# Performance work log

Hardware: AMD Instinct MI355X
Metric: run time of the kernel (lower is better)

Reference implementation:

```python
import jax, jax.numpy as jnp
import numpy as np


def setup_inputs() -> dict:
    key = jax.random.key(0)
    k1, k2, k3, k4 = jax.random.split(key, 4)
    N = 100000          # n_users + n_items nodes
    E = 1600000         # nonzeros in normalized adjacency (avg degree 16)
    D = 64              # embedding dim
    edge_row = jnp.sort(jax.random.randint(k1, (E,), 0, N, dtype=jnp.int32))
    edge_col = jax.random.randint(k2, (E,), 0, N, dtype=jnp.int32)
    edge_val = jax.random.uniform(k3, (E,), dtype=jnp.float32)
    embeds = jax.random.normal(k4, (N, D), dtype=jnp.float32)
    return {
        "edge_row": edge_row,
        "edge_col": edge_col,
        "edge_val": edge_val,
        "embeds": embeds,
        "num_nodes": N,
    }


def reference(edge_row, edge_col, edge_val, embeds, num_nodes):
    # out = A @ embeds, A given in COO: A[row[e], col[e]] = val[e]
    gathered = edge_val[:, None] * embeds[edge_col]        # [E, D]
    out = jax.ops.segment_sum(gathered, edge_row, num_segments=num_nodes)  # [N, D]
    return out
```

## Files before the change

kernel.cpp:

```cpp
#include <hip/hip_runtime.h>


#define GCN_D 64

typedef float f4 __attribute__((ext_vector_type(4)));

__global__ __launch_bounds__(256) void quant_kernel(
    const float* __restrict__ embeds,
    unsigned char* __restrict__ ebq,
    float* __restrict__ scale,
    int N)
{
    const int t   = blockIdx.x * blockDim.x + threadIdx.x;
    const int row = t >> 3;
    if (row >= N) return;
    const int l8 = (threadIdx.x & 7) * 8;

    const f4 a = __builtin_nontemporal_load(
        (const f4*)(embeds + (size_t)row * GCN_D + l8));
    const f4 b = __builtin_nontemporal_load(
        (const f4*)(embeds + (size_t)row * GCN_D + l8 + 4));

    float m = fmaxf(fmaxf(fmaxf(fabsf(a.x), fabsf(a.y)),
                          fmaxf(fabsf(a.z), fabsf(a.w))),
                    fmaxf(fmaxf(fabsf(b.x), fabsf(b.y)),
                          fmaxf(fabsf(b.z), fabsf(b.w))));
    m = fmaxf(m, __shfl_xor(m, 1));
    m = fmaxf(m, __shfl_xor(m, 2));
    m = fmaxf(m, __shfl_xor(m, 4));

    const float inv = (m > 0.f) ? 127.f / m : 0.f;
    const int q0 = (int)rintf(fminf(fmaxf(a.x * inv, -127.f), 127.f)) + 128;
    const int q1 = (int)rintf(fminf(fmaxf(a.y * inv, -127.f), 127.f)) + 128;
    const int q2 = (int)rintf(fminf(fmaxf(a.z * inv, -127.f), 127.f)) + 128;
    const int q3 = (int)rintf(fminf(fmaxf(a.w * inv, -127.f), 127.f)) + 128;
    const int q4 = (int)rintf(fminf(fmaxf(b.x * inv, -127.f), 127.f)) + 128;
    const int q5 = (int)rintf(fminf(fmaxf(b.y * inv, -127.f), 127.f)) + 128;
    const int q6 = (int)rintf(fminf(fmaxf(b.z * inv, -127.f), 127.f)) + 128;
    const int q7 = (int)rintf(fminf(fmaxf(b.w * inv, -127.f), 127.f)) + 128;

    unsigned int p0 =
        (unsigned)q0 | ((unsigned)q1 << 8) | ((unsigned)q2 << 16) | ((unsigned)q3 << 24);
    unsigned int p1 =
        (unsigned)q4 | ((unsigned)q5 << 8) | ((unsigned)q6 << 16) | ((unsigned)q7 << 24);

    unsigned int* dst = (unsigned int*)(ebq + (size_t)row * GCN_D + l8);
    dst[0] = p0;
    dst[1] = p1;
    if ((threadIdx.x & 7) == 0) scale[row] = m * (1.f / 127.f);
}

__global__ __launch_bounds__(256) void edge_kernel(
    const int* __restrict__ edge_row,
    const int* __restrict__ edge_col,
    const float* __restrict__ edge_val,
    const float* __restrict__ scale,
    int* __restrict__ row_ptr,
    int2* __restrict__ pw,
    int E, int N)
{
    const int e = blockIdx.x * blockDim.x + threadIdx.x;
    if (e >= E) return;
    const int r    = edge_row[e];
    const int prev = (e == 0) ? -1 : edge_row[e - 1];
    for (int k = prev + 1; k <= r; ++k) row_ptr[k] = e;
    if (e == E - 1)
        for (int k = r + 1; k <= N; ++k) row_ptr[k] = E;

    const int   c = edge_col[e];
    const float w = edge_val[e] * scale[c];
    pw[e] = make_int2(c, __float_as_int(w));
}

__device__ __forceinline__ void q8_fma4(unsigned int g, float w, f4& acc) {
    acc.x += w * (float)( g        & 0xffu);
    acc.y += w * (float)((g >> 8)  & 0xffu);
    acc.z += w * (float)((g >> 16) & 0xffu);
    acc.w += w * (float)( g >> 24);
}

__global__ __launch_bounds__(256) void gcn_row_q8_kernel(
    const int* __restrict__ row_ptr,
    const int2* __restrict__ pw,
    const unsigned char* __restrict__ ebq,
    float* __restrict__ out,
    int N)
{
    const int tid = blockIdx.x * blockDim.x + threadIdx.x;
    const int row = tid >> 4;
    if (row >= N) return;
    const int db = (threadIdx.x & 15) * 4;

    const int p0 = row_ptr[row];
    const int p1 = row_ptr[row + 1];

    f4    acc = (f4)0.0f;
    float ws  = 0.0f;

    if (p1 > p0) {
        const int nb = (p1 - p0 + 7) >> 3;
        int k = p0;

        int      cA[8], cB[8];
        float    wA[8], wB[8];
        unsigned gA[8], gB[8];

        auto LOAD = [&](int kk, int* c, float* w, unsigned* g) {
            #pragma unroll
            for (int j = 0; j < 8; ++j) {
                const int idx = (kk + j < p1) ? (kk + j) : (p1 - 1);
                const int2 t  = pw[idx];
                c[j] = t.x;
                w[j] = (kk + j < p1) ? __int_as_float(t.y) : 0.0f;
            }
            #pragma unroll
            for (int j = 0; j < 8; ++j)
                g[j] = *(const unsigned*)(ebq + (size_t)c[j] * GCN_D + db);
        };
        auto COMP = [&](const float* w, const unsigned* g) {
            #pragma unroll
            for (int j = 0; j < 8; ++j) {
                q8_fma4(g[j], w[j], acc);
                ws += w[j];
            }
        };

        LOAD(k, cA, wA, gA); k += 8;
        int b = 1;
        for (; b + 1 < nb; b += 2) {
            LOAD(k, cB, wB, gB); k += 8;
            COMP(wA, gA);
            LOAD(k, cA, wA, gA); k += 8;
            COMP(wB, gB);
        }
        if (b < nb) {
            LOAD(k, cB, wB, gB);
            COMP(wA, gA);
            COMP(wB, gB);
        } else {
            COMP(wA, gA);
        }
    }

    acc = acc - 128.0f * ws;
    __builtin_nontemporal_store(acc, (f4*)(out + (size_t)row * GCN_D + db));
}

extern "C" void kernel_launch(void* const* d_in, const int* in_sizes, int n_in,
                              void* d_out, int out_size, void* d_ws, size_t ws_size,
                              hipStream_t stream) {
    const int*   edge_row = (const int*)d_in[0];
    const int*   edge_col = (const int*)d_in[1];
    const float* edge_val = (const float*)d_in[2];
    const float* embeds   = (const float*)d_in[3];
    float*       out      = (float*)d_out;

    const int E = in_sizes[0];
    const int N = out_size / GCN_D;

    int* row_ptr = (int*)d_ws;
    const size_t sc_off = (((size_t)(N + 1) * 4) + 255) & ~(size_t)255;
    float* scale = (float*)((char*)d_ws + sc_off);
    const size_t pw_off = ((sc_off + (size_t)N * 4) + 255) & ~(size_t)255;
    int2* pw = (int2*)((char*)d_ws + pw_off);
    const size_t q_off = ((pw_off + (size_t)E * 8) + 255) & ~(size_t)255;
    unsigned char* ebq = (unsigned char*)d_ws + q_off;

    const int quant_blocks = (N * 8 + 255) / 256;
    quant_kernel<<<quant_blocks, 256, 0, stream>>>(embeds, ebq, scale, N);

    const int edge_blocks = (E + 255) / 256;
    edge_kernel<<<edge_blocks, 256, 0, stream>>>(
        edge_row, edge_col, edge_val, scale, row_ptr, pw, E, N);

    const int row_blocks = (N * 16 + 255) / 256;
    gcn_row_q8_kernel<<<row_blocks, 256, 0, stream>>>(
        row_ptr, pw, ebq, out, N);
}
```

Before: 139.6 us.

## Switch gather table from int8 to bf16 and fuse prep kernels

```diff
diff --git a/kernel.cpp b/kernel.cpp
--- a/kernel.cpp
+++ b/kernel.cpp
@@ -4,137 +4,114 @@
 #define GCN_D 64
 
 typedef float f4 __attribute__((ext_vector_type(4)));
+typedef unsigned int u2 __attribute__((ext_vector_type(2)));
+typedef unsigned int uv4 __attribute__((ext_vector_type(4)));
 
-__global__ __launch_bounds__(256) void quant_kernel(
-    const float* __restrict__ embeds,
-    unsigned char* __restrict__ ebq,
-    float* __restrict__ scale,
-    int N)
-{
-    const int t   = blockIdx.x * blockDim.x + threadIdx.x;
-    const int row = t >> 3;
-    if (row >= N) return;
-    const int l8 = (threadIdx.x & 7) * 8;
-
-    const f4 a = __builtin_nontemporal_load(
-        (const f4*)(embeds + (size_t)row * GCN_D + l8));
-    const f4 b = __builtin_nontemporal_load(
-        (const f4*)(embeds + (size_t)row * GCN_D + l8 + 4));
-
-    float m = fmaxf(fmaxf(fmaxf(fabsf(a.x), fabsf(a.y)),
-                          fmaxf(fabsf(a.z), fabsf(a.w))),
-                    fmaxf(fmaxf(fabsf(b.x), fabsf(b.y)),
-                          fmaxf(fabsf(b.z), fabsf(b.w))));
-    m = fmaxf(m, __shfl_xor(m, 1));
-    m = fmaxf(m, __shfl_xor(m, 2));
-    m = fmaxf(m, __shfl_xor(m, 4));
-
-    const float inv = (m > 0.f) ? 127.f / m : 0.f;
-    const int q0 = (int)rintf(fminf(fmaxf(a.x * inv, -127.f), 127.f)) + 128;
-    const int q1 = (int)rintf(fminf(fmaxf(a.y * inv, -127.f), 127.f)) + 128;
-    const int q2 = (int)rintf(fminf(fmaxf(a.z * inv, -127.f), 127.f)) + 128;
-    const int q3 = (int)rintf(fminf(fmaxf(a.w * inv, -127.f), 127.f)) + 128;
-    const int q4 = (int)rintf(fminf(fmaxf(b.x * inv, -127.f), 127.f)) + 128;
-    const int q5 = (int)rintf(fminf(fmaxf(b.y * inv, -127.f), 127.f)) + 128;
-    const int q6 = (int)rintf(fminf(fmaxf(b.z * inv, -127.f), 127.f)) + 128;
-    const int q7 = (int)rintf(fminf(fmaxf(b.w * inv, -127.f), 127.f)) + 128;
-
-    unsigned int p0 =
-        (unsigned)q0 | ((unsigned)q1 << 8) | ((unsigned)q2 << 16) | ((unsigned)q3 << 24);
-    unsigned int p1 =
-        (unsigned)q4 | ((unsigned)q5 << 8) | ((unsigned)q6 << 16) | ((unsigned)q7 << 24);
-
-    unsigned int* dst = (unsigned int*)(ebq + (size_t)row * GCN_D + l8);
-    dst[0] = p0;
-    dst[1] = p1;
-    if ((threadIdx.x & 7) == 0) scale[row] = m * (1.f / 127.f);
+__device__ __forceinline__ unsigned bf16rne_pack(float lo, float hi) {
+    unsigned ul = __float_as_uint(lo);
+    unsigned uh = __float_as_uint(hi);
+    ul = (ul + 0x7fffu + ((ul >> 16) & 1u)) >> 16;
+    uh = (uh + 0x7fffu + ((uh >> 16) & 1u)) & 0xffff0000u;
+    return ul | uh;
 }
 
-__global__ __launch_bounds__(256) void edge_kernel(
-    const int* __restrict__ edge_row,
+__global__ __launch_bounds__(256) void prep_kernel(
+    const float* __restrict__ embeds,
+    unsigned char* __restrict__ ebb,
+    int quant_blocks,
+    const int* __restrict__ edge_row, int* __restrict__ row_ptr, int E, int N)
+{
+    if ((int)blockIdx.x < quant_blocks) {
+        const int t   = blockIdx.x * blockDim.x + threadIdx.x;
+        const int row = t >> 3;
+        if (row >= N) return;
+        const int l8 = (threadIdx.x & 7) * 8;
+
+        const f4 a = __builtin_nontemporal_load(
+            (const f4*)(embeds + (size_t)row * GCN_D + l8));
+        const f4 b = __builtin_nontemporal_load(
+            (const f4*)(embeds + (size_t)row * GCN_D + l8 + 4));
+
+        uv4 p;
+        p.x = bf16rne_pack(a.x, a.y);
+        p.y = bf16rne_pack(a.z, a.w);
+        p.z = bf16rne_pack(b.x, b.y);
+        p.w = bf16rne_pack(b.z, b.w);
+
+        *(uv4*)(ebb + (size_t)row * (GCN_D * 2) + l8 * 2) = p;
+    } else {
+        const int e = (blockIdx.x - quant_blocks) * blockDim.x + threadIdx.x;
+        if (e >= E) return;
+        const int r    = edge_row[e];
+        const int prev = (e == 0) ? -1 : edge_row[e - 1];
+        for (int k = prev + 1; k <= r; ++k) row_ptr[k] = e;
+        if (e == E - 1)
+            for (int k = r + 1; k <= N; ++k) row_ptr[k] = E;
+    }
+}
+
+__global__ __launch_bounds__(256) void gcn_row_bf16_kernel(
+    const int* __restrict__ row_ptr,
     const int* __restrict__ edge_col,
     const float* __restrict__ edge_val,
-    const float* __restrict__ scale,
-    int* __restrict__ row_ptr,
-    int2* __restrict__ pw,
-    int E, int N)
-{
-    const int e = blockIdx.x * blockDim.x + threadIdx.x;
-    if (e >= E) return;
-    const int r    = edge_row[e];
-    const int prev = (e == 0) ? -1 : edge_row[e - 1];
-    for (int k = prev + 1; k <= r; ++k) row_ptr[k] = e;
-    if (e == E - 1)
-        for (int k = r + 1; k <= N; ++k) row_ptr[k] = E;
-
-    const int   c = edge_col[e];
-    const float w = edge_val[e] * scale[c];
-    pw[e] = make_int2(c, __float_as_int(w));
-}
-
-__device__ __forceinline__ void q8_fma4(unsigned int g, float w, f4& acc) {
-    acc.x += w * (float)( g        & 0xffu);
-    acc.y += w * (float)((g >> 8)  & 0xffu);
-    acc.z += w * (float)((g >> 16) & 0xffu);
-    acc.w += w * (float)( g >> 24);
-}
-
-__global__ __launch_bounds__(256) void gcn_row_q8_kernel(
-    const int* __restrict__ row_ptr,
-    const int2* __restrict__ pw,
-    const unsigned char* __restrict__ ebq,
+    const unsigned char* __restrict__ ebb,
     float* __restrict__ out,
     int N)
 {
     const int tid = blockIdx.x * blockDim.x + threadIdx.x;
     const int row = tid >> 4;
     if (row >= N) return;
-    const int db = (threadIdx.x & 15) * 4;
+    const int off = (threadIdx.x & 15) * 8;
+    const int db  = (threadIdx.x & 15) * 4;
 
     const int p0 = row_ptr[row];
     const int p1 = row_ptr[row + 1];
 
-    f4    acc = (f4)0.0f;
-    float ws  = 0.0f;
+    f4 acc = (f4)0.0f;
 
     if (p1 > p0) {
         const int nb = (p1 - p0 + 7) >> 3;
         int k = p0;
 
-        int      cA[8], cB[8];
-        float    wA[8], wB[8];
-        unsigned gA[8], gB[8];
+        float wA[8], wB[8];
+        u2    gA[8], gB[8];
 
-        auto LOAD = [&](int kk, int* c, float* w, unsigned* g) {
+        auto LOAD = [&](int kk, float* w, u2* g) {
+            int c[8];
             #pragma unroll
             for (int j = 0; j < 8; ++j) {
                 const int idx = (kk + j < p1) ? (kk + j) : (p1 - 1);
-                const int2 t  = pw[idx];
-                c[j] = t.x;
-                w[j] = (kk + j < p1) ? __int_as_float(t.y) : 0.0f;
+                c[j] = edge_col[idx];
+                w[j] = (kk + j < p1) ? edge_val[idx] : 0.0f;
             }
             #pragma unroll
             for (int j = 0; j < 8; ++j)
-                g[j] = *(const unsigned*)(ebq + (size_t)c[j] * GCN_D + db);
+                g[j] = *(const u2*)(ebb + (size_t)c[j] * (GCN_D * 2) + off);
         };
-        auto COMP = [&](const float* w, const unsigned* g) {
+        auto COMP = [&](const float* w, const u2* g) {
             #pragma unroll
             for (int j = 0; j < 8; ++j) {
-                q8_fma4(g[j], w[j], acc);
-                ws += w[j];
+                const float x0 = __uint_as_float(g[j].x << 16);
+                const float x1 = __uint_as_float(g[j].x & 0xffff0000u);
+                const float x2 = __uint_as_float(g[j].y << 16);
+                const float x3 = __uint_as_float(g[j].y & 0xffff0000u);
+                acc.x = fmaf(w[j], x0, acc.x);
+                acc.y = fmaf(w[j], x1, acc.y);
+                acc.z = fmaf(w[j], x2, acc.z);
+                acc.w = fmaf(w[j], x3, acc.w);
             }
         };
 
-        LOAD(k, cA, wA, gA); k += 8;
+        LOAD(k, wA, gA); k += 8;
         int b = 1;
         for (; b + 1 < nb; b += 2) {
-            LOAD(k, cB, wB, gB); k += 8;
+            LOAD(k, wB, gB); k += 8;
             COMP(wA, gA);
-            LOAD(k, cA, wA, gA); k += 8;
+            LOAD(k, wA, gA); k += 8;
             COMP(wB, gB);
         }
         if (b < nb) {
-            LOAD(k, cB, wB, gB);
+            LOAD(k, wB, gB);
             COMP(wA, gA);
             COMP(wB, gB);
         } else {
@@ -142,7 +119,6 @@
         }
     }
 
-    acc = acc - 128.0f * ws;
     __builtin_nontemporal_store(acc, (f4*)(out + (size_t)row * GCN_D + db));
 }
 
@@ -159,21 +135,15 @@
     const int N = out_size / GCN_D;
 
     int* row_ptr = (int*)d_ws;
-    const size_t sc_off = (((size_t)(N + 1) * 4) + 255) & ~(size_t)255;
-    float* scale = (float*)((char*)d_ws + sc_off);
-    const size_t pw_off = ((sc_off + (size_t)N * 4) + 255) & ~(size_t)255;
-    int2* pw = (int2*)((char*)d_ws + pw_off);
-    const size_t q_off = ((pw_off + (size_t)E * 8) + 255) & ~(size_t)255;
-    unsigned char* ebq = (unsigned char*)d_ws + q_off;
+    const size_t tb_off = (((size_t)(N + 1) * 4) + 255) & ~(size_t)255;
+    unsigned char* ebb = (unsigned char*)d_ws + tb_off;
 
     const int quant_blocks = (N * 8 + 255) / 256;
-    quant_kernel<<<quant_blocks, 256, 0, stream>>>(embeds, ebq, scale, N);
-
-    const int edge_blocks = (E + 255) / 256;
-    edge_kernel<<<edge_blocks, 256, 0, stream>>>(
-        edge_row, edge_col, edge_val, scale, row_ptr, pw, E, N);
+    const int rp_blocks    = (E + 255) / 256;
+    prep_kernel<<<quant_blocks + rp_blocks, 256, 0, stream>>>(
+        embeds, ebb, quant_blocks, edge_row, row_ptr, E, N);
 
     const int row_blocks = (N * 16 + 255) / 256;
-    gcn_row_q8_kernel<<<row_blocks, 256, 0, stream>>>(
-        row_ptr, pw, ebq, out, N);
+    gcn_row_bf16_kernel<<<row_blocks, 256, 0, stream>>>(
+        row_ptr, edge_col, edge_val, ebb, out, N);
 }
```

Result: no change. 137.1 us (-1.8%).
